# Kernel optimization log

Hardware: AMD Instinct MI355X
Metric: run time of the kernel (lower is better)

## Reference

```python
import jax, jax.numpy as jnp
import numpy as np

B, N, M = 2, 2048, 2048
D_K, D_V, H = 256, 256, 8
D_KS = D_K // H  # 32, per-head key dim (ceil(256/8))
D_VS = D_V // H  # 32
MASK_BIG = 1e32


def setup_inputs() -> dict:
    key = jax.random.key(0)
    ks = jax.random.split(key, 10)
    s = 0.02
    queries = jax.random.normal(ks[0], (B, N, D_K), jnp.float32)
    keys_ = jax.random.normal(ks[1], (B, M, D_K), jnp.float32)
    values = jax.random.normal(ks[2], (B, M, D_V), jnp.float32)
    presence = (jax.random.uniform(ks[3], (B, M)) > 0.3).astype(jnp.float32)
    Wq = jax.random.normal(ks[4], (D_K, D_KS * H), jnp.float32) * s
    bq = jnp.zeros((D_KS * H,), jnp.float32)
    Wk = jax.random.normal(ks[5], (D_K, D_KS * H), jnp.float32) * s
    bk = jnp.zeros((D_KS * H,), jnp.float32)
    Wv = jax.random.normal(ks[6], (D_V, D_VS * H), jnp.float32) * s
    bv = jnp.zeros((D_VS * H,), jnp.float32)
    Wo = jax.random.normal(ks[7], (D_VS * H, D_V), jnp.float32) * s
    bo = jnp.zeros((D_V,), jnp.float32)
    return {"queries": queries, "keys": keys_, "values": values, "presence": presence,
            "Wq": Wq, "bq": bq, "Wk": Wk, "bk": bk, "Wv": Wv, "bv": bv, "Wo": Wo, "bo": bo}


def reference(queries, keys, values, presence, Wq, bq, Wk, bk, Wv, bv, Wo, bo):
    # Project and split into heads. torch's split(d_k_s,-1)+cat(...,0) puts the
    # head index as the outer batch dim; a [B,N,H,d] reshape is the same math.
    q = (queries @ Wq + bq).reshape(B, N, H, D_KS)
    k = (keys @ Wk + bk).reshape(B, M, H, D_KS)
    v = (values @ Wv + bv).reshape(B, M, H, D_VS)
    # Raw scores, additive presence mask, then scale by sqrt(per-head d_k)
    scores = jnp.einsum('bnhd,bmhd->bhnm', q, k)
    scores = scores - (1.0 - presence)[:, None, None, :] * MASK_BIG
    attn = jax.nn.softmax(scores / np.sqrt(D_KS).astype(np.float32), axis=-1)
    o = jnp.einsum('bhnm,bmhd->bnhd', attn, v).reshape(B, N, H * D_VS)
    return o @ Wo + bo
```

## Files before the change

kernel.cpp:

```cpp
#include <hip/hip_runtime.h>

#define B_ 2
#define N_ 2048
#define M_ 2048
#define D_ 256
#define H_ 8
#define DH_ 32
#define SPLITS 2
#define QSCALE (0.17677669529663689f * 1.4426950408889634f)

typedef __attribute__((ext_vector_type(8))) short short8;
typedef __attribute__((ext_vector_type(4))) float f32x4;
typedef unsigned short u16;
typedef unsigned int u32;

#if __has_builtin(__builtin_amdgcn_exp2f)
#define EXP2 __builtin_amdgcn_exp2f
#else
#define EXP2 exp2f
#endif

__device__ __forceinline__ u16 f2bf(float f) {
  u32 u = __float_as_uint(f);
  return (u16)((u + 0x7fffu + ((u >> 16) & 1u)) >> 16);
}
__device__ __forceinline__ u32 cvtpk_bf16(float lo, float hi) {
  u32 r;
  asm("v_cvt_pk_bf16_f32 %0, %1, %2" : "=v"(r) : "v"(lo), "v"(hi));
  return r;
}
__device__ __forceinline__ void gload_lds16(const u16* g, u16* l) {
  __builtin_amdgcn_global_load_lds((const __attribute__((address_space(1))) void*)g,
                                   (__attribute__((address_space(3))) void*)l, 16, 0, 0);
}

__global__ __launch_bounds__(256, 2) void qkvproj_kernel(
    const float* __restrict__ Xq, const float* __restrict__ Xk, const float* __restrict__ Xv,
    const float* __restrict__ Wq, const float* __restrict__ Wk, const float* __restrict__ Wv,
    const float* __restrict__ bq, const float* __restrict__ bk, const float* __restrict__ bv,
    u16* __restrict__ qb, u16* __restrict__ kb, u16* __restrict__ vtb) {
  __shared__ u16 wsT[64 * 256];
  __shared__ u16 xs[64 * 256];
  const int p = blockIdx.y;
  const int nb = blockIdx.x & 63, cb = blockIdx.x >> 6;
  const int n0B = nb * 64, c0B = cb * 64;
  const float* X = p == 0 ? Xq : (p == 1 ? Xk : Xv);
  const float* W = p == 0 ? Wq : (p == 1 ? Wk : Wv);
  const float* bias = p == 0 ? bq : (p == 1 ? bk : bv);
  const int t = threadIdx.x;

  {
    const int cL = (t & 15) * 4, kB = (t >> 4) * 16;
    const float* wp = W + (size_t)kB * D_ + c0B + cL;
#pragma unroll
    for (int u = 0; u < 4; ++u) {
      const int k0 = kB + 4 * u;
      const f32x4 w0 = *(const f32x4*)(wp + (size_t)(4 * u + 0) * D_);
      const f32x4 w1 = *(const f32x4*)(wp + (size_t)(4 * u + 1) * D_);
      const f32x4 w2 = *(const f32x4*)(wp + (size_t)(4 * u + 2) * D_);
      const f32x4 w3 = *(const f32x4*)(wp + (size_t)(4 * u + 3) * D_);
#pragma unroll
      for (int cc = 0; cc < 4; ++cc) {
        const int c = cL + cc;
        uint2 v;
        v.x = cvtpk_bf16(w0[cc], w1[cc]);
        v.y = cvtpk_bf16(w2[cc], w3[cc]);
        *(uint2*)(wsT + c * 256 + (((k0 >> 3) ^ (c & 7)) * 8) + (k0 & 7)) = v;
      }
    }
  }
  {
    const int nL = t >> 2, k64 = (t & 3) * 64;
    const float* xp = X + (size_t)(n0B + nL) * D_ + k64;
#pragma unroll
    for (int m = 0; m < 8; ++m) {
      const f32x4 a = *(const f32x4*)(xp + 8 * m);
      const f32x4 b = *(const f32x4*)(xp + 8 * m + 4);
      uint4 v;
      v.x = cvtpk_bf16(a[0], a[1]);
      v.y = cvtpk_bf16(a[2], a[3]);
      v.z = cvtpk_bf16(b[0], b[1]);
      v.w = cvtpk_bf16(b[2], b[3]);
      const int k0 = k64 + 8 * m;
      *(uint4*)(xs + nL * 256 + (((k0 >> 3) ^ (nL & 7)) * 8)) = v;
    }
  }
  __syncthreads();

  const int wv = t >> 6, lane = t & 63, lr = lane & 15, lg = lane >> 4;
  const f32x4 zz = {0.f, 0.f, 0.f, 0.f};
  f32x4 acc[4] = {zz, zz, zz, zz};
  const int arow = wv * 16 + lr;
#pragma unroll
  for (int ks = 0; ks < 8; ++ks) {
    const short8 a = *(const short8*)(wsT + arow * 256 + (((ks * 4 + lg) ^ (arow & 7)) * 8));
#pragma unroll
    for (int ng = 0; ng < 4; ++ng) {
      const int brow = ng * 16 + lr;
      const short8 b = *(const short8*)(xs + brow * 256 + (((ks * 4 + lg) ^ (brow & 7)) * 8));
      acc[ng] = __builtin_amdgcn_mfma_f32_16x16x32_bf16(a, b, acc[ng], 0, 0, 0);
    }
  }

  const int cg4 = c0B + wv * 16 + lg * 4;
  const f32x4 bias4 = *(const f32x4*)(bias + cg4);
  if (p < 2) {
    u16* ob = p == 0 ? qb : kb;
    const float sc = p == 0 ? QSCALE : 1.0f;
#pragma unroll
    for (int ng = 0; ng < 4; ++ng) {
      const int n = n0B + ng * 16 + lr;
      const int b = n >> 11, nn = n & (N_ - 1);
#pragma unroll
      for (int j = 0; j < 4; ++j) {
        const int c = cg4 + j;
        ob[((size_t)(b * H_ + (c >> 5)) * N_ + nn) * DH_ + (c & 31)] =
            f2bf((acc[ng][j] + bias4[j]) * sc);
      }
    }
  } else {
#pragma unroll
    for (int ng = 0; ng < 4; ++ng) {
      const int n = n0B + ng * 16 + lr;
      const int b = n >> 11, nn = n & (M_ - 1);
#pragma unroll
      for (int j = 0; j < 4; ++j) {
        const int c = cg4 + j;
        vtb[((size_t)(b * H_ + (c >> 5)) * DH_ + (c & 31)) * M_ + nn] =
            f2bf(acc[ng][j] + bias4[j]);
      }
    }
  }
}

__global__ __launch_bounds__(256, 4) void attn_kernel(
    const u16* __restrict__ qb, const u16* __restrict__ kb,
    const u16* __restrict__ vtb, const float* __restrict__ presence,
    float* __restrict__ opart, float* __restrict__ lpart) {
  __shared__ u16 kvlds[2][4096];
  __shared__ u16 plds[4][1024];
  const int t = threadIdx.x;
  const int wv = t >> 6, lane = t & 63;
  const int lr = lane & 15, lg = lane >> 4;
  const int s = blockIdx.x >> 9;
  const int bh = (blockIdx.x >> 5) & 15;
  const int qblk = blockIdx.x & 31;
  const int b = bh >> 3, h = bh & 7;
  const int n0 = qblk * 64 + wv * 16;
  const int m0 = s * (M_ / SPLITS);
  const int NI = (M_ / SPLITS) / 64;

  const int gsk = (t & 3) ^ ((t >> 3) & 3);
  const u16* kst = kb + ((size_t)bh * M_ + m0 + (t >> 2)) * DH_ + gsk * 8;
  const int gsv = (t & 7) ^ ((t >> 3) & 7);
  const u16* vst = vtb + ((size_t)bh * DH_ + (t >> 3)) * M_ + m0 + gsv * 8;
  u16* const ldswK = &kvlds[0][0] + wv * 512;
  u16* const ldswV = &kvlds[0][0] + 2048 + wv * 512;

  const int ko0 = lr * 32 + (lg ^ ((lr >> 1) & 3)) * 8;
  const int sw = lr & 7;
  const int vo0 = (lg ^ sw) * 8;
  const int vo1 = ((4 + lg) ^ sw) * 8;

  const short8 qf = *(const short8*)(qb + ((size_t)bh * N_ + n0 + lr) * DH_ + lg * 8);
  const float* pbase = presence + (size_t)b * M_ + m0 + lg * 4;
  u16* const plw = plds[wv] + lr * 64;

  const f32x4 zz = {0.f, 0.f, 0.f, 0.f};
  f32x4 o0 = zz, o1 = zz, racc = zz;

  gload_lds16(kst, ldswK);
  gload_lds16(vst, ldswV);
  __syncthreads();

#pragma unroll 2
  for (int i = 0; i < NI; ++i) {
    const int mm = i * 64;
    const u16* kl = &kvlds[i & 1][0];
    const u16* vl = &kvlds[i & 1][2048];
    f32x4 pr[4];
#pragma unroll
    for (int tt = 0; tt < 4; ++tt) pr[tt] = *(const f32x4*)(pbase + mm + tt * 16);
    if (i + 1 < NI) {
      const int bo = ((i + 1) & 1) * 4096;
      gload_lds16(kst + (size_t)(i + 1) * (64 * DH_), ldswK + bo);
      gload_lds16(vst + (size_t)(i + 1) * 64, ldswV + bo);
    }

    f32x4 s4[4];
    __builtin_amdgcn_s_setprio(1);
#pragma unroll
    for (int tt = 0; tt < 4; ++tt) {
      const short8 kf = *(const short8*)(kl + tt * 512 + ko0);
      s4[tt] = __builtin_amdgcn_mfma_f32_16x16x32_bf16(kf, qf, zz, 0, 0, 0);
    }
    __builtin_amdgcn_s_setprio(0);

#pragma unroll
    for (int tt = 0; tt < 4; ++tt) {
      s4[tt] += (pr[tt] - 1.f) * 1e30f;
#pragma unroll
      for (int j = 0; j < 4; ++j) s4[tt][j] = EXP2(s4[tt][j]);
      racc += s4[tt];
      const int slot = (2 * tt + (lg >> 1)) ^ sw;
      *(uint2*)(plw + slot * 8 + (lg & 1) * 4) =
          make_uint2(cvtpk_bf16(s4[tt][0], s4[tt][1]), cvtpk_bf16(s4[tt][2], s4[tt][3]));
    }
    const short8 pf0 = *(const short8*)(plw + vo0);
    const short8 pf1 = *(const short8*)(plw + vo1);
    const short8 vf0 = *(const short8*)(vl + lr * 64 + vo0);
    const short8 vf1 = *(const short8*)(vl + lr * 64 + vo1);
    const short8 vf2 = *(const short8*)(vl + (16 + lr) * 64 + vo0);
    const short8 vf3 = *(const short8*)(vl + (16 + lr) * 64 + vo1);
    __builtin_amdgcn_s_setprio(1);
    o0 = __builtin_amdgcn_mfma_f32_16x16x32_bf16(pf0, vf0, o0, 0, 0, 0);
    o0 = __builtin_amdgcn_mfma_f32_16x16x32_bf16(pf1, vf1, o0, 0, 0, 0);
    o1 = __builtin_amdgcn_mfma_f32_16x16x32_bf16(pf0, vf2, o1, 0, 0, 0);
    o1 = __builtin_amdgcn_mfma_f32_16x16x32_bf16(pf1, vf3, o1, 0, 0, 0);
    __builtin_amdgcn_s_setprio(0);
    __syncthreads();
  }

  float l = (racc[0] + racc[1]) + (racc[2] + racc[3]);
  l += __shfl_xor(l, 16);
  l += __shfl_xor(l, 32);
  if (lg == 0) lpart[((size_t)s * (B_ * N_) + b * N_ + n0 + lr) * H_ + h] = l;

  float* ob = opart + ((size_t)s * (B_ * N_) + (size_t)b * N_ + n0) * D_ + h * DH_;
#pragma unroll
  for (int j = 0; j < 4; ++j) {
    const int q = lg * 4 + j;
    ob[(size_t)q * D_ + lr] = o0[j];
    ob[(size_t)q * D_ + 16 + lr] = o1[j];
  }
}

__global__ __launch_bounds__(256, 2) void projo_kernel(
    const float* __restrict__ opart, const float* __restrict__ lpart,
    const float* __restrict__ Wo, const float* __restrict__ bo,
    float* __restrict__ out) {
  __shared__ u16 wsT[64 * 256];
  __shared__ u16 xs[64 * 256];
  const int nb = blockIdx.x & 63, cb = blockIdx.x >> 6;
  const int n0B = nb * 64, c0B = cb * 64;
  const int t = threadIdx.x;

  {
    const int cL = (t & 15) * 4, kB = (t >> 4) * 16;
    const float* wp = Wo + (size_t)kB * D_ + c0B + cL;
#pragma unroll
    for (int u = 0; u < 4; ++u) {
      const int k0 = kB + 4 * u;
      const f32x4 w0 = *(const f32x4*)(wp + (size_t)(4 * u + 0) * D_);
      const f32x4 w1 = *(const f32x4*)(wp + (size_t)(4 * u + 1) * D_);
      const f32x4 w2 = *(const f32x4*)(wp + (size_t)(4 * u + 2) * D_);
      const f32x4 w3 = *(const f32x4*)(wp + (size_t)(4 * u + 3) * D_);
#pragma unroll
      for (int cc = 0; cc < 4; ++cc) {
        const int c = cL + cc;
        uint2 v;
        v.x = cvtpk_bf16(w0[cc], w1[cc]);
        v.y = cvtpk_bf16(w2[cc], w3[cc]);
        *(uint2*)(wsT + c * 256 + (((k0 >> 3) ^ (c & 7)) * 8) + (k0 & 7)) = v;
      }
    }
  }
  {
    const int nL = t >> 2, k64 = (t & 3) * 64;
    const int gn = n0B + nL;
    const float* o0p = opart + (size_t)gn * D_ + k64;
    const float* o1p = o0p + (size_t)(B_ * N_) * D_;
    const int h0 = k64 >> 5;
    const float il0 = 1.f / (lpart[(size_t)gn * H_ + h0] +
                             lpart[((size_t)(B_ * N_) + gn) * H_ + h0]);
    const float il1 = 1.f / (lpart[(size_t)gn * H_ + h0 + 1] +
                             lpart[((size_t)(B_ * N_) + gn) * H_ + h0 + 1]);
#pragma unroll
    for (int m = 0; m < 8; ++m) {
      f32x4 a = *(const f32x4*)(o0p + 8 * m) + *(const f32x4*)(o1p + 8 * m);
      f32x4 b = *(const f32x4*)(o0p + 8 * m + 4) + *(const f32x4*)(o1p + 8 * m + 4);
      const float il = (m < 4) ? il0 : il1;
      a *= il;
      b *= il;
      uint4 v;
      v.x = cvtpk_bf16(a[0], a[1]);
      v.y = cvtpk_bf16(a[2], a[3]);
      v.z = cvtpk_bf16(b[0], b[1]);
      v.w = cvtpk_bf16(b[2], b[3]);
      const int k0 = k64 + 8 * m;
      *(uint4*)(xs + nL * 256 + (((k0 >> 3) ^ (nL & 7)) * 8)) = v;
    }
  }
  __syncthreads();

  const int wv = t >> 6, lane = t & 63, lr = lane & 15, lg = lane >> 4;
  const f32x4 zz = {0.f, 0.f, 0.f, 0.f};
  f32x4 acc[4] = {zz, zz, zz, zz};
  const int arow = wv * 16 + lr;
#pragma unroll
  for (int ks = 0; ks < 8; ++ks) {
    const short8 a = *(const short8*)(xs + arow * 256 + (((ks * 4 + lg) ^ (arow & 7)) * 8));
#pragma unroll
    for (int ng = 0; ng < 4; ++ng) {
      const int brow = ng * 16 + lr;
      const short8 bfr = *(const short8*)(wsT + brow * 256 + (((ks * 4 + lg) ^ (brow & 7)) * 8));
      acc[ng] = __builtin_amdgcn_mfma_f32_16x16x32_bf16(a, bfr, acc[ng], 0, 0, 0);
    }
  }
#pragma unroll
  for (int ng = 0; ng < 4; ++ng) {
    const int c = c0B + ng * 16 + lr;
    const float bb = bo[c];
#pragma unroll
    for (int j = 0; j < 4; ++j)
      out[(size_t)(n0B + wv * 16 + lg * 4 + j) * D_ + c] = acc[ng][j] + bb;
  }
}

extern "C" void kernel_launch(void* const* d_in, const int* in_sizes, int n_in,
                              void* d_out, int out_size, void* d_ws, size_t ws_size,
                              hipStream_t stream) {
  (void)in_sizes; (void)n_in; (void)out_size; (void)ws_size;
  const float* queries  = (const float*)d_in[0];
  const float* keys     = (const float*)d_in[1];
  const float* values   = (const float*)d_in[2];
  const float* presence = (const float*)d_in[3];
  const float* Wq = (const float*)d_in[4];
  const float* bq = (const float*)d_in[5];
  const float* Wk = (const float*)d_in[6];
  const float* bk = (const float*)d_in[7];
  const float* Wv = (const float*)d_in[8];
  const float* bv = (const float*)d_in[9];
  const float* Wo = (const float*)d_in[10];
  const float* bo = (const float*)d_in[11];

  u16* qb  = (u16*)d_ws;
  u16* kb  = qb + (size_t)B_ * H_ * N_ * DH_;
  u16* vtb = kb + (size_t)B_ * H_ * M_ * DH_;
  float* opart = (float*)(vtb + (size_t)B_ * H_ * DH_ * M_);
  float* lpart = opart + (size_t)SPLITS * B_ * N_ * D_;

  qkvproj_kernel<<<dim3(256, 3), 256, 0, stream>>>(
      queries, keys, values, Wq, Wk, Wv, bq, bk, bv, qb, kb, vtb);
  attn_kernel<<<SPLITS * 16 * 32, 256, 0, stream>>>(qb, kb, vtb, presence, opart, lpart);
  projo_kernel<<<256, 256, 0, stream>>>(opart, lpart, Wo, bo, (float*)d_out);
}
```

Baseline: 47.57 us.

## Process two query fragments per wave, use four KV splits, stage presence in LDS

Each attention wave now computes 32 query rows against every staged K/V tile instead of 16, so each block covers 128 queries and K/V LDS loads are reused across twice as many queries. To keep the grid size unchanged, the key dimension is split four ways instead of two, and the output projection now sums four partial outputs and partial normalizers. The presence mask is loaded once per block into LDS and applied by multiplying after exp2, rather than as an additive bias before it. The trade-off is a larger partial-output workspace and more read traffic in the projection kernel, plus higher register pressure in the attention loop.

```diff
diff --git a/kernel.cpp b/kernel.cpp
--- a/kernel.cpp
+++ b/kernel.cpp
@@ -6,7 +6,7 @@
 #define D_ 256
 #define H_ 8
 #define DH_ 32
-#define SPLITS 2
+#define SPLITS 4
 #define QSCALE (0.17677669529663689f * 1.4426950408889634f)
 
 typedef __attribute__((ext_vector_type(8))) short short8;
@@ -30,6 +30,10 @@
   return r;
 }
 __device__ __forceinline__ void gload_lds16(const u16* g, u16* l) {
+  __builtin_amdgcn_global_load_lds((const __attribute__((address_space(1))) void*)g,
+                                   (__attribute__((address_space(3))) void*)l, 16, 0, 0);
+}
+__device__ __forceinline__ void gload_lds16f(const float* g, float* l) {
   __builtin_amdgcn_global_load_lds((const __attribute__((address_space(1))) void*)g,
                                    (__attribute__((address_space(3))) void*)l, 16, 0, 0);
 }
@@ -75,12 +79,12 @@
 #pragma unroll
     for (int m = 0; m < 8; ++m) {
       const f32x4 a = *(const f32x4*)(xp + 8 * m);
-      const f32x4 b = *(const f32x4*)(xp + 8 * m + 4);
+      const f32x4 b2 = *(const f32x4*)(xp + 8 * m + 4);
       uint4 v;
       v.x = cvtpk_bf16(a[0], a[1]);
       v.y = cvtpk_bf16(a[2], a[3]);
-      v.z = cvtpk_bf16(b[0], b[1]);
-      v.w = cvtpk_bf16(b[2], b[3]);
+      v.z = cvtpk_bf16(b2[0], b2[1]);
+      v.w = cvtpk_bf16(b2[2], b2[3]);
       const int k0 = k64 + 8 * m;
       *(uint4*)(xs + nL * 256 + (((k0 >> 3) ^ (nL & 7)) * 8)) = v;
     }
@@ -138,15 +142,17 @@
     const u16* __restrict__ vtb, const float* __restrict__ presence,
     float* __restrict__ opart, float* __restrict__ lpart) {
   __shared__ u16 kvlds[2][4096];
-  __shared__ u16 plds[4][1024];
+  __shared__ u16 plds[4][2048];
+  __shared__ float prlds[512];
   const int t = threadIdx.x;
   const int wv = t >> 6, lane = t & 63;
   const int lr = lane & 15, lg = lane >> 4;
-  const int s = blockIdx.x >> 9;
-  const int bh = (blockIdx.x >> 5) & 15;
-  const int qblk = blockIdx.x & 31;
+  const int g = blockIdx.x;
+  const int s = g >> 8;
+  const int bh = (g >> 4) & 15;
+  const int qblk = g & 15;
   const int b = bh >> 3, h = bh & 7;
-  const int n0 = qblk * 64 + wv * 16;
+  const int n0 = qblk * 128 + wv * 32;
   const int m0 = s * (M_ / SPLITS);
   const int NI = (M_ / SPLITS) / 64;
 
@@ -162,15 +168,19 @@
   const int vo0 = (lg ^ sw) * 8;
   const int vo1 = ((4 + lg) ^ sw) * 8;
 
-  const short8 qf = *(const short8*)(qb + ((size_t)bh * N_ + n0 + lr) * DH_ + lg * 8);
-  const float* pbase = presence + (size_t)b * M_ + m0 + lg * 4;
-  u16* const plw = plds[wv] + lr * 64;
+  const u16* qbase = qb + ((size_t)bh * N_ + n0 + lr) * DH_ + lg * 8;
+  const short8 qf0 = *(const short8*)(qbase);
+  const short8 qf1 = *(const short8*)(qbase + 16 * DH_);
+  u16* const plw0 = plds[wv] + lr * 64;
+  u16* const plw1 = plds[wv] + 1024 + lr * 64;
 
   const f32x4 zz = {0.f, 0.f, 0.f, 0.f};
-  f32x4 o0 = zz, o1 = zz, racc = zz;
+  f32x4 o0 = zz, o1 = zz, o2 = zz, o3 = zz, racc0 = zz, racc1 = zz;
 
   gload_lds16(kst, ldswK);
   gload_lds16(vst, ldswV);
+  if (wv < 2)
+    gload_lds16f(presence + (size_t)b * M_ + m0 + wv * 256 + lane * 4, prlds + wv * 256);
   __syncthreads();
 
 #pragma unroll 2
@@ -178,53 +188,70 @@
     const int mm = i * 64;
     const u16* kl = &kvlds[i & 1][0];
     const u16* vl = &kvlds[i & 1][2048];
-    f32x4 pr[4];
-#pragma unroll
-    for (int tt = 0; tt < 4; ++tt) pr[tt] = *(const f32x4*)(pbase + mm + tt * 16);
     if (i + 1 < NI) {
       const int bo = ((i + 1) & 1) * 4096;
       gload_lds16(kst + (size_t)(i + 1) * (64 * DH_), ldswK + bo);
       gload_lds16(vst + (size_t)(i + 1) * 64, ldswV + bo);
     }
 
-    f32x4 s4[4];
+    f32x4 s4a[4], s4b[4];
     __builtin_amdgcn_s_setprio(1);
 #pragma unroll
     for (int tt = 0; tt < 4; ++tt) {
       const short8 kf = *(const short8*)(kl + tt * 512 + ko0);
-      s4[tt] = __builtin_amdgcn_mfma_f32_16x16x32_bf16(kf, qf, zz, 0, 0, 0);
+      s4a[tt] = __builtin_amdgcn_mfma_f32_16x16x32_bf16(kf, qf0, zz, 0, 0, 0);
+      s4b[tt] = __builtin_amdgcn_mfma_f32_16x16x32_bf16(kf, qf1, zz, 0, 0, 0);
     }
     __builtin_amdgcn_s_setprio(0);
 
 #pragma unroll
     for (int tt = 0; tt < 4; ++tt) {
-      s4[tt] += (pr[tt] - 1.f) * 1e30f;
-#pragma unroll
-      for (int j = 0; j < 4; ++j) s4[tt][j] = EXP2(s4[tt][j]);
-      racc += s4[tt];
-      const int slot = (2 * tt + (lg >> 1)) ^ sw;
-      *(uint2*)(plw + slot * 8 + (lg & 1) * 4) =
-          make_uint2(cvtpk_bf16(s4[tt][0], s4[tt][1]), cvtpk_bf16(s4[tt][2], s4[tt][3]));
-    }
-    const short8 pf0 = *(const short8*)(plw + vo0);
-    const short8 pf1 = *(const short8*)(plw + vo1);
+      const f32x4 pr = *(const f32x4*)(prlds + mm + tt * 16 + lg * 4);
+      const int so = (((2 * tt + (lg >> 1)) ^ sw) * 8) + (lg & 1) * 4;
+#pragma unroll
+      for (int j = 0; j < 4; ++j) s4a[tt][j] = EXP2(s4a[tt][j]);
+      s4a[tt] *= pr;
+      racc0 += s4a[tt];
+      *(uint2*)(plw0 + so) =
+          make_uint2(cvtpk_bf16(s4a[tt][0], s4a[tt][1]), cvtpk_bf16(s4a[tt][2], s4a[tt][3]));
+#pragma unroll
+      for (int j = 0; j < 4; ++j) s4b[tt][j] = EXP2(s4b[tt][j]);
+      s4b[tt] *= pr;
+      racc1 += s4b[tt];
+      *(uint2*)(plw1 + so) =
+          make_uint2(cvtpk_bf16(s4b[tt][0], s4b[tt][1]), cvtpk_bf16(s4b[tt][2], s4b[tt][3]));
+    }
+    const short8 pf00 = *(const short8*)(plw0 + vo0);
+    const short8 pf01 = *(const short8*)(plw0 + vo1);
+    const short8 pf10 = *(const short8*)(plw1 + vo0);
+    const short8 pf11 = *(const short8*)(plw1 + vo1);
     const short8 vf0 = *(const short8*)(vl + lr * 64 + vo0);
     const short8 vf1 = *(const short8*)(vl + lr * 64 + vo1);
     const short8 vf2 = *(const short8*)(vl + (16 + lr) * 64 + vo0);
     const short8 vf3 = *(const short8*)(vl + (16 + lr) * 64 + vo1);
     __builtin_amdgcn_s_setprio(1);
-    o0 = __builtin_amdgcn_mfma_f32_16x16x32_bf16(pf0, vf0, o0, 0, 0, 0);
-    o0 = __builtin_amdgcn_mfma_f32_16x16x32_bf16(pf1, vf1, o0, 0, 0, 0);
-    o1 = __builtin_amdgcn_mfma_f32_16x16x32_bf16(pf0, vf2, o1, 0, 0, 0);
-    o1 = __builtin_amdgcn_mfma_f32_16x16x32_bf16(pf1, vf3, o1, 0, 0, 0);
+    o0 = __builtin_amdgcn_mfma_f32_16x16x32_bf16(pf00, vf0, o0, 0, 0, 0);
+    o0 = __builtin_amdgcn_mfma_f32_16x16x32_bf16(pf01, vf1, o0, 0, 0, 0);
+    o1 = __builtin_amdgcn_mfma_f32_16x16x32_bf16(pf00, vf2, o1, 0, 0, 0);
+    o1 = __builtin_amdgcn_mfma_f32_16x16x32_bf16(pf01, vf3, o1, 0, 0, 0);
+    o2 = __builtin_amdgcn_mfma_f32_16x16x32_bf16(pf10, vf0, o2, 0, 0, 0);
+    o2 = __builtin_amdgcn_mfma_f32_16x16x32_bf16(pf11, vf1, o2, 0, 0, 0);
+    o3 = __builtin_amdgcn_mfma_f32_16x16x32_bf16(pf10, vf2, o3, 0, 0, 0);
+    o3 = __builtin_amdgcn_mfma_f32_16x16x32_bf16(pf11, vf3, o3, 0, 0, 0);
     __builtin_amdgcn_s_setprio(0);
     __syncthreads();
   }
 
-  float l = (racc[0] + racc[1]) + (racc[2] + racc[3]);
-  l += __shfl_xor(l, 16);
-  l += __shfl_xor(l, 32);
-  if (lg == 0) lpart[((size_t)s * (B_ * N_) + b * N_ + n0 + lr) * H_ + h] = l;
+  float l0 = (racc0[0] + racc0[1]) + (racc0[2] + racc0[3]);
+  l0 += __shfl_xor(l0, 16);
+  l0 += __shfl_xor(l0, 32);
+  float l1 = (racc1[0] + racc1[1]) + (racc1[2] + racc1[3]);
+  l1 += __shfl_xor(l1, 16);
+  l1 += __shfl_xor(l1, 32);
+  if (lg == 0) {
+    lpart[((size_t)s * (B_ * N_) + b * N_ + n0 + lr) * H_ + h] = l0;
+    lpart[((size_t)s * (B_ * N_) + b * N_ + n0 + 16 + lr) * H_ + h] = l1;
+  }
 
   float* ob = opart + ((size_t)s * (B_ * N_) + (size_t)b * N_ + n0) * D_ + h * DH_;
 #pragma unroll
@@ -232,6 +259,8 @@
     const int q = lg * 4 + j;
     ob[(size_t)q * D_ + lr] = o0[j];
     ob[(size_t)q * D_ + 16 + lr] = o1[j];
+    ob[(size_t)(16 + q) * D_ + lr] = o2[j];
+    ob[(size_t)(16 + q) * D_ + 16 + lr] = o3[j];
   }
 }
 
@@ -268,25 +297,33 @@
   {
     const int nL = t >> 2, k64 = (t & 3) * 64;
     const int gn = n0B + nL;
-    const float* o0p = opart + (size_t)gn * D_ + k64;
-    const float* o1p = o0p + (size_t)(B_ * N_) * D_;
     const int h0 = k64 >> 5;
-    const float il0 = 1.f / (lpart[(size_t)gn * H_ + h0] +
-                             lpart[((size_t)(B_ * N_) + gn) * H_ + h0]);
-    const float il1 = 1.f / (lpart[(size_t)gn * H_ + h0 + 1] +
-                             lpart[((size_t)(B_ * N_) + gn) * H_ + h0 + 1]);
+    float l0s = 0.f, l1s = 0.f;
+#pragma unroll
+    for (int sp = 0; sp < SPLITS; ++sp) {
+      l0s += lpart[((size_t)sp * (B_ * N_) + gn) * H_ + h0];
+      l1s += lpart[((size_t)sp * (B_ * N_) + gn) * H_ + h0 + 1];
+    }
+    const float il0 = 1.f / l0s, il1 = 1.f / l1s;
+    const float* obase = opart + (size_t)gn * D_ + k64;
 #pragma unroll
     for (int m = 0; m < 8; ++m) {
-      f32x4 a = *(const f32x4*)(o0p + 8 * m) + *(const f32x4*)(o1p + 8 * m);
-      f32x4 b = *(const f32x4*)(o0p + 8 * m + 4) + *(const f32x4*)(o1p + 8 * m + 4);
+      f32x4 a = {0.f, 0.f, 0.f, 0.f};
+      f32x4 b2 = {0.f, 0.f, 0.f, 0.f};
+#pragma unroll
+      for (int sp = 0; sp < SPLITS; ++sp) {
+        const float* op = obase + (size_t)sp * (B_ * N_) * D_;
+        a += *(const f32x4*)(op + 8 * m);
+        b2 += *(const f32x4*)(op + 8 * m + 4);
+      }
       const float il = (m < 4) ? il0 : il1;
       a *= il;
-      b *= il;
+      b2 *= il;
       uint4 v;
       v.x = cvtpk_bf16(a[0], a[1]);
       v.y = cvtpk_bf16(a[2], a[3]);
-      v.z = cvtpk_bf16(b[0], b[1]);
-      v.w = cvtpk_bf16(b[2], b[3]);
+      v.z = cvtpk_bf16(b2[0], b2[1]);
+      v.w = cvtpk_bf16(b2[2], b2[3]);
       const int k0 = k64 + 8 * m;
       *(uint4*)(xs + nL * 256 + (((k0 >> 3) ^ (nL & 7)) * 8)) = v;
     }
@@ -342,6 +379,6 @@
 
   qkvproj_kernel<<<dim3(256, 3), 256, 0, stream>>>(
       queries, keys, values, Wq, Wk, Wv, bq, bk, bv, qb, kb, vtb);
-  attn_kernel<<<SPLITS * 16 * 32, 256, 0, stream>>>(qb, kb, vtb, presence, opart, lpart);
+  attn_kernel<<<SPLITS * 16 * 16, 256, 0, stream>>>(qb, kb, vtb, presence, opart, lpart);
   projo_kernel<<<256, 256, 0, stream>>>(opart, lpart, Wo, bo, (float*)d_out);
 }
```

New measurement: 49.44 us. 3.9% more time.
